# Performance work log

Hardware: AMD Instinct MI355X
Metric: run time of the kernel (lower is better)

The kernel has to match this reference:

```python
import jax, jax.numpy as jnp
import numpy as np

EPS = 1e-5


def _conv1x1(x, w, b):
    # x: (B,C,H,W), w: (O,C), b: (O,)
    return jnp.einsum('oc,bchw->bohw', w, x) + b[None, :, None, None]


def _attn(q, k, v):
    # q,k: (B,Dq,H,W); v: (B,C,H,W). Full NxN attention, softmax over keys.
    B, _, H, W = q.shape
    N = H * W
    Q = q.reshape(B, -1, N)
    K = k.reshape(B, -1, N)
    V = v.reshape(B, -1, N)
    A = jax.nn.softmax(jnp.einsum('bci,bcj->bij', Q, K), axis=-1)  # (B,N,N)
    out = jnp.einsum('bcj,bij->bci', V, A)  # out[b,c,i] = sum_j V[b,c,j] A[b,i,j]
    return out.reshape(B, -1, H, W)


def _std(feat):
    # torch.var(dim=2) is unbiased (ddof=1)
    B, C = feat.shape[:2]
    v = jnp.var(feat.reshape(B, C, -1), axis=2, ddof=1) + EPS
    return jnp.sqrt(v)[:, :, None, None]


def _fmm(fb_feat, bg_feat):
    return fb_feat * (_std(bg_feat) / _std(fb_feat))


def setup_inputs() -> dict:
    key = jax.random.key(0)
    ks = jax.random.split(key, 16)
    B, C, H, W = 2, 256, 64, 64
    D = C // 8
    s = 0.05
    inp = {
        'x': jax.random.normal(ks[0], (B, C, H, W), jnp.float32),
        'mask': jax.random.randint(ks[1], (B, 1, H, W), 0, 2).astype(jnp.float32),
        'sa_wq': jax.random.normal(ks[2], (D, C), jnp.float32) * s,
        'sa_bq': jax.random.normal(ks[3], (D,), jnp.float32) * s,
        'sa_wk': jax.random.normal(ks[4], (D, C), jnp.float32) * s,
        'sa_bk': jax.random.normal(ks[5], (D,), jnp.float32) * s,
        'sa_wv': jax.random.normal(ks[6], (C, C), jnp.float32) * s,
        'sa_bv': jax.random.normal(ks[7], (C,), jnp.float32) * s,
        'sa_gamma': jax.random.uniform(ks[8], (1,), jnp.float32),
        'wq': jax.random.normal(ks[9], (D, C), jnp.float32) * s,
        'bq': jax.random.normal(ks[10], (D,), jnp.float32) * s,
        'wk': jax.random.normal(ks[11], (D, C), jnp.float32) * s,
        'bk': jax.random.normal(ks[12], (D,), jnp.float32) * s,
        'wv': jax.random.normal(ks[13], (C, C), jnp.float32) * s,
        'bv': jax.random.normal(ks[14], (C,), jnp.float32) * s,
        'gamma': jax.random.uniform(ks[15], (1,), jnp.float32),
    }
    return inp


def reference(x, mask, sa_wq, sa_bq, sa_wk, sa_bk, sa_wv, sa_bv, sa_gamma,
              wq, bq, wk, bk, wv, bv, gamma):
    # --- Self_Attn ---
    sa_out = _attn(_conv1x1(x, sa_wq, sa_bq),
                   _conv1x1(x, sa_wk, sa_bk),
                   _conv1x1(x, sa_wv, sa_bv))
    x = sa_gamma[0] * sa_out + x
    # --- FB_FMM masked cross attention (mask already at feature resolution) ---
    reverse_mask = 1.0 - mask
    feature_b = reverse_mask * x
    feature_f = mask * x
    sw_bg = _attn(_conv1x1(feature_f, wq, bq),
                  _conv1x1(feature_b, wk, bk),
                  _conv1x1(feature_b, wv, bv))
    out = x + gamma[0] * _fmm(feature_f, sw_bg)
    return out
```

## Files before the change

kernel.cpp:

```cpp
#include <hip/hip_runtime.h>
#include <stdint.h>

typedef _Float16 f16;
typedef __attribute__((ext_vector_type(8))) _Float16 half8;
typedef __attribute__((ext_vector_type(2))) __fp16 fp16x2;
typedef __attribute__((ext_vector_type(8))) short short8;
typedef __attribute__((ext_vector_type(4))) float f32x4;

#define NPOS 4096
#define CCH  256
#define OQK  64
#define BATCH 2
#define NSPLIT 4
#define KEYS_PER_SPLIT 1024
#define NT (KEYS_PER_SPLIT / 64)

typedef __attribute__((address_space(3))) uint32_t lds_u32;
typedef __attribute__((address_space(1))) const uint32_t glb_u32;

__device__ __forceinline__ float bf2f(short u) {
    union { uint32_t i; float f; } c;
    c.i = ((uint32_t)(uint16_t)u) << 16;
    return c.f;
}
__device__ __forceinline__ short f2bf(float f) {
    union { float f; uint32_t i; } c; c.f = f;
    uint32_t lsb = (c.i >> 16) & 1u;
    c.i += 0x7FFFu + lsb;
    return (short)(c.i >> 16);
}

__device__ __forceinline__ bool detect_bf16(const uint32_t* mw) {
    int hits = 0;
    #pragma unroll
    for (int i = 0; i < 64; ++i) hits += ((mw[i] & 0xFFFFu) == 0x3F80u) ? 1 : 0;
    return hits != 0;
}

__device__ __forceinline__ void load8(const void* base, size_t e0, bool bf, float* v) {
    if (bf) {
        short8 s = *(const short8*)((const short*)base + e0);
        #pragma unroll
        for (int j = 0; j < 8; ++j) v[j] = bf2f(s[j]);
    } else {
        const float* fp = (const float*)base + e0;
        float4 a = *(const float4*)fp;
        float4 b = *(const float4*)(fp + 4);
        v[0] = a.x; v[1] = a.y; v[2] = a.z; v[3] = a.w;
        v[4] = b.x; v[5] = b.y; v[6] = b.z; v[7] = b.w;
    }
}
__device__ __forceinline__ float load1(const void* base, int i, bool bf) {
    return bf ? bf2f(((const short*)base)[i]) : ((const float*)base)[i];
}

__device__ __forceinline__ int pkrtz(float a, float b) {
    union { fp16x2 h; int i; } u;
    u.h = __builtin_amdgcn_cvt_pkrtz(a, b);
    return u.i;
}

__global__ __launch_bounds__(256) void convert_inputs(
    const uint32_t* __restrict__ mask_raw,
    const void* __restrict__ w1q, const void* __restrict__ w1k, const void* __restrict__ w1v_,
    const void* __restrict__ b1q, const void* __restrict__ b1k, const void* __restrict__ b1v_,
    const void* __restrict__ g1,
    const void* __restrict__ w2q, const void* __restrict__ w2k, const void* __restrict__ w2v_,
    const void* __restrict__ b2q, const void* __restrict__ b2k, const void* __restrict__ b2v_,
    const void* __restrict__ g2,
    float* __restrict__ maskf,
    f16* __restrict__ w1qk, f16* __restrict__ w1vm, f16* __restrict__ b1,
    f16* __restrict__ w2qk, f16* __restrict__ w2vm, f16* __restrict__ b2,
    float* __restrict__ gam)
{
    const bool bf = detect_bf16(mask_raw);
    const int blk = blockIdx.x, tid = threadIdx.x;
    float v[8];
    if (blk < 4) {
        const size_t e0 = ((size_t)blk * 256 + tid) * 8;
        load8(mask_raw, e0, bf, v);
        float4 f0 = {v[0], v[1], v[2], v[3]}, f1 = {v[4], v[5], v[6], v[7]};
        *(float4*)(maskf + e0) = f0;
        *(float4*)(maskf + e0 + 4) = f1;
    } else if (blk < 12) {
        const size_t g = ((size_t)(blk - 4) * 256 + tid) * 8;
        const int o = (int)(g >> 8), cc = (int)(g & 255);
        const void* src = (o < 32) ? w1q : w1k;
        const size_t se = (size_t)((o < 32) ? o : o - 32) * 256 + cc;
        load8(src, se, bf, v);
        half8 h;
        #pragma unroll
        for (int j = 0; j < 8; ++j) h[j] = (f16)v[j];
        *(half8*)(w1qk + g) = h;
    } else if (blk < 44) {
        const size_t g = ((size_t)(blk - 12) * 256 + tid) * 8;
        load8(w1v_, g, bf, v);
        half8 h;
        #pragma unroll
        for (int j = 0; j < 8; ++j) h[j] = (f16)v[j];
        *(half8*)(w1vm + g) = h;
    } else if (blk < 52) {
        const size_t g = ((size_t)(blk - 44) * 256 + tid) * 8;
        const int o = (int)(g >> 8), cc = (int)(g & 255);
        const void* src = (o < 32) ? w2q : w2k;
        const size_t se = (size_t)((o < 32) ? o : o - 32) * 256 + cc;
        load8(src, se, bf, v);
        half8 h;
        #pragma unroll
        for (int j = 0; j < 8; ++j) h[j] = (f16)v[j];
        *(half8*)(w2qk + g) = h;
    } else if (blk < 84) {
        const size_t g = ((size_t)(blk - 52) * 256 + tid) * 8;
        load8(w2v_, g, bf, v);
        half8 h;
        #pragma unroll
        for (int j = 0; j < 8; ++j) h[j] = (f16)v[j];
        *(half8*)(w2vm + g) = h;
    } else {
        for (int i = tid; i < 320; i += 256) {
            const void* s1 = (i < 32) ? b1q : (i < 64) ? b1k : b1v_;
            const void* s2 = (i < 32) ? b2q : (i < 64) ? b2k : b2v_;
            const int ii = (i < 32) ? i : (i < 64) ? i - 32 : i - 64;
            b1[i] = (f16)load1(s1, ii, bf);
            b2[i] = (f16)load1(s2, ii, bf);
        }
        if (tid == 0) {
            gam[0] = load1(g1, 0, bf);
            gam[1] = load1(g2, 0, bf);
        }
    }
}

__global__ __launch_bounds__(256) void conv_qkv(
    const void* __restrict__ xin, int is_raw,
    const uint32_t* __restrict__ mask_raw,
    const f16* __restrict__ wqk,
    const f16* __restrict__ wvm,
    const f16* __restrict__ bias,
    const float* __restrict__ maskf, int use_mask,
    f16* __restrict__ qkout,
    f16* __restrict__ vout)
{
    const bool bf = is_raw ? detect_bf16(mask_raw) : false;
    const int b    = blockIdx.y;
    const int n0   = blockIdx.x * 32;
    const int tid  = threadIdx.x;
    const int lane = tid & 63;
    const int w    = tid >> 6;
    const int lo   = lane & 15;
    const int hi   = lane >> 4;

    __shared__ f16 xt[32 * 256];

    {
        const int nc = tid & 3;
        const int cg = tid >> 2;
        #pragma unroll
        for (int it = 0; it < 4; ++it) {
            const int c = cg + 64 * it;
            const size_t off = ((size_t)b * CCH + c) * NPOS + n0 + nc * 8;
            float v8[8];
            load8(xin, off, bf, v8);
            #pragma unroll
            for (int j = 0; j < 8; ++j) {
                const int n = nc * 8 + j;
                int byte = n * 512 + c * 2;
                byte ^= ((n & 7) << 4);
                *(f16*)((char*)xt + byte) = (f16)v8[j];
            }
        }
    }
    __syncthreads();

    const f32x4 z = {0.f, 0.f, 0.f, 0.f};
    f32x4 acc_qk[2];
    f32x4 acc_v[4][2];
    #pragma unroll
    for (int i = 0; i < 2; ++i) {
        acc_qk[i] = z;
        #pragma unroll
        for (int j = 0; j < 4; ++j) acc_v[j][i] = z;
    }

    #pragma unroll 1
    for (int ks = 0; ks < 8; ++ks) {
        const int ce = ks * 32 + 8 * hi;
        half8 xfr[2];
        #pragma unroll
        for (int nt = 0; nt < 2; ++nt) {
            const int n = nt * 16 + lo;
            int byte = n * 512 + ce * 2;
            byte ^= ((n & 7) << 4);
            xfr[nt] = *(const half8*)((const char*)xt + byte);
        }
        {
            half8 wf = *(const half8*)(wqk + (size_t)(w * 16 + lo) * 256 + ce);
            #pragma unroll
            for (int nt = 0; nt < 2; ++nt)
                acc_qk[nt] = __builtin_amdgcn_mfma_f32_16x16x32_f16(xfr[nt], wf, acc_qk[nt], 0, 0, 0);
        }
        #pragma unroll
        for (int ot = 0; ot < 4; ++ot) {
            half8 wf = *(const half8*)(wvm + (size_t)(w * 64 + ot * 16 + lo) * 256 + ce);
            #pragma unroll
            for (int nt = 0; nt < 2; ++nt)
                acc_v[ot][nt] = __builtin_amdgcn_mfma_f32_16x16x32_f16(wf, xfr[nt], acc_v[ot][nt], 0, 0, 0);
        }
    }

    {
        const int o = w * 16 + lo;
        const float bb = (float)bias[o];
        #pragma unroll
        for (int nt = 0; nt < 2; ++nt) {
            #pragma unroll
            for (int r = 0; r < 4; ++r) {
                const int n = n0 + nt * 16 + 4 * hi + r;
                float mult = 1.f;
                if (use_mask) {
                    const float mv = maskf[b * NPOS + n];
                    mult = (o < 32) ? mv : (1.f - mv);
                }
                qkout[((size_t)b * NPOS + n) * OQK + o] = (f16)(mult * acc_qk[nt][r] + bb);
            }
        }
    }
    {
        float mv_n[2];
        #pragma unroll
        for (int nt = 0; nt < 2; ++nt)
            mv_n[nt] = use_mask ? (1.f - maskf[b * NPOS + n0 + nt * 16 + lo]) : 1.f;
        #pragma unroll
        for (int ot = 0; ot < 4; ++ot) {
            #pragma unroll
            for (int r = 0; r < 4; ++r) {
                const int oc = w * 64 + ot * 16 + 4 * hi + r;
                const float bb = (float)bias[64 + oc];
                #pragma unroll
                for (int nt = 0; nt < 2; ++nt) {
                    const int n = n0 + nt * 16 + lo;
                    vout[((size_t)b * CCH + oc) * NPOS + n] = (f16)(mv_n[nt] * acc_v[ot][nt][r] + bb);
                }
            }
        }
    }
}

__global__ __launch_bounds__(512, 4) void attn_split(
    const f16* __restrict__ qk,
    const f16* __restrict__ vbuf,
    f16* __restrict__ po,
    float2* __restrict__ pml)
{
    const int id    = blockIdx.x;
    const int xg    = id & 7;
    const int split = xg & 3;
    const int b     = xg >> 2;
    const int q0    = (id >> 3) * 64;
    const int tid   = threadIdx.x;
    const int lane  = tid & 63;
    const int w     = tid >> 6;
    const int lo    = lane & 15;
    const int hi    = lane >> 4;
    const int qown  = (w & 3) * 16;
    const int cbase = w * 32;

    __shared__ f16 kv[CCH * 64];
    __shared__ f16 kbuf[2][64 * 64];
    __shared__ f16 plds[64 * 64];
    __shared__ float sc_lds[64];
    __shared__ float l_lds[64];
    __shared__ int   flag_lds[4];

    const int trow = tid >> 3;
    const int tch  = tid & 7;

    half8 qfrag;
    if (w < 4)
        qfrag = *(const half8*)(qk + ((size_t)b * NPOS + q0 + qown + lo) * OQK + 8 * hi);

    const f32x4 z = {0.f, 0.f, 0.f, 0.f};
    f32x4 acc[2][4];
    #pragma unroll
    for (int i = 0; i < 2; ++i)
        #pragma unroll
        for (int j = 0; j < 4; ++j) acc[i][j] = z;
    float m_run = -3.0e38f, l_run = 0.f;

    const f16* vsrc = vbuf + (size_t)b * CCH * NPOS;
    const f16* ksrc = qk + (size_t)b * NPOS * OQK;

    #define STAGE_V(kt)                                                        \
    {                                                                          \
        const int j0s = split * KEYS_PER_SPLIT + (kt) * 64;                    \
        _Pragma("unroll")                                                      \
        for (int i = 0; i < 4; ++i) {                                          \
            const int c = i * 64 + trow;                                       \
            const f16* g = vsrc + (size_t)c * NPOS + j0s + ((tch ^ (c & 7)) * 8); \
            char* d = (char*)kv + i * 8192 + w * 1024;                         \
            __builtin_amdgcn_global_load_lds((glb_u32*)g, (lds_u32*)d, 16, 0, 0); \
        }                                                                      \
    }
    #define STAGE_K(kt)                                                        \
    {                                                                          \
        const int j0s = split * KEYS_PER_SPLIT + (kt) * 64;                    \
        char* kb = (char*)kbuf + ((kt) & 1) * 8192;                            \
        const f16* g = ksrc + (size_t)(j0s + trow) * OQK + ((tch ^ (trow & 7)) * 8); \
        __builtin_amdgcn_global_load_lds((glb_u32*)g, (lds_u32*)(kb + w * 1024), 16, 0, 0); \
    }

    STAGE_V(0)
    STAGE_K(0)
    STAGE_K(1)
    asm volatile("s_waitcnt vmcnt(1)" ::: "memory");
    __builtin_amdgcn_s_barrier();
    asm volatile("" ::: "memory");

    #pragma unroll 1
    for (int kt = 0; kt < NT; ++kt) {
        if (w < 4) {
            const char* kb = (const char*)kbuf + (kt & 1) * 8192;
            f32x4 s[4];
            __builtin_amdgcn_s_setprio(1);
            #pragma unroll
            for (int jt = 0; jt < 4; ++jt) {
                const int krow = jt * 16 + lo;
                const half8 kfrag = *(const half8*)(kb + krow * 128
                                                    + ((64 + hi * 16) ^ ((krow & 7) << 4)));
                s[jt] = __builtin_amdgcn_mfma_f32_16x16x32_f16(kfrag, qfrag, z, 0, 0, 0);
            }
            __builtin_amdgcn_s_setprio(0);
            float pm = s[0][0];
            #pragma unroll
            for (int jt = 0; jt < 4; ++jt)
                #pragma unroll
                for (int r = 0; r < 4; ++r) pm = fmaxf(pm, s[jt][r]);
            pm = fmaxf(pm, __shfl_xor(pm, 16, 64));
            pm = fmaxf(pm, __shfl_xor(pm, 32, 64));
            const bool g = __any(pm - m_run > 8.f);
            float scv = 1.f;
            if (g) {
                const float mnew = fmaxf(m_run, pm);
                scv = __expf(m_run - mnew);
                m_run = mnew;
                l_run *= scv;
            }
            float rs = 0.f;
            #pragma unroll
            for (int jt = 0; jt < 4; ++jt) {
                #pragma unroll
                for (int r = 0; r < 4; ++r) {
                    const float pv = __expf(s[jt][r] - m_run);
                    s[jt][r] = pv;
                    rs += pv;
                }
            }
            rs += __shfl_xor(rs, 16, 64);
            rs += __shfl_xor(rs, 32, 64);
            l_run += rs;
            const int q = qown + lo;
            #pragma unroll
            for (int jt = 0; jt < 4; ++jt) {
                union { int i2[2]; uint64_t u; } pw;
                pw.i2[0] = pkrtz(s[jt][0], s[jt][1]);
                pw.i2[1] = pkrtz(s[jt][2], s[jt][3]);
                *(uint64_t*)((char*)plds + q * 128 + ((jt * 32 + 8 * hi) ^ ((q & 7) << 4))) = pw.u;
            }
            if (hi == 0) sc_lds[q] = scv;
            if (lane == 0) flag_lds[w] = g ? 1 : 0;
        }

        asm volatile("s_waitcnt lgkmcnt(0)" ::: "memory");
        if (kt + 1 < NT) {
            asm volatile("s_waitcnt vmcnt(1)" ::: "memory");
        } else {
            asm volatile("s_waitcnt vmcnt(0)" ::: "memory");
        }
        __builtin_amdgcn_sched_barrier(0);
        __builtin_amdgcn_s_barrier();
        asm volatile("" ::: "memory");

        #pragma unroll
        for (int qt = 0; qt < 4; ++qt) {
            if (flag_lds[qt]) {
                const float sc = sc_lds[qt * 16 + lo];
                #pragma unroll
                for (int ct = 0; ct < 2; ++ct) acc[ct][qt] *= sc;
            }
        }
        __builtin_amdgcn_s_setprio(1);
        #pragma unroll
        for (int ksp = 0; ksp < 2; ++ksp) {
            half8 pf[4];
            #pragma unroll
            for (int qt = 0; qt < 4; ++qt)
                pf[qt] = *(const half8*)((const char*)plds + (qt * 16 + lo) * 128
                                         + ((ksp * 64 + 16 * hi) ^ ((lo & 7) << 4)));
            #pragma unroll
            for (int ct = 0; ct < 2; ++ct) {
                const int vrow = cbase + ct * 16 + lo;
                const half8 vf = *(const half8*)((const char*)kv + vrow * 128
                                                 + ((ksp * 64 + 16 * hi) ^ ((vrow & 7) << 4)));
                #pragma unroll
                for (int qt = 0; qt < 4; ++qt)
                    acc[ct][qt] = __builtin_amdgcn_mfma_f32_16x16x32_f16(vf, pf[qt], acc[ct][qt], 0, 0, 0);
            }
        }
        __builtin_amdgcn_s_setprio(0);

        asm volatile("s_waitcnt lgkmcnt(0) vmcnt(0)" ::: "memory");
        __builtin_amdgcn_sched_barrier(0);
        __builtin_amdgcn_s_barrier();
        asm volatile("" ::: "memory");
        if (kt + 1 < NT) STAGE_V(kt + 1)
        if (kt + 2 < NT) STAGE_K(kt + 2)
    }
    #undef STAGE_K
    #undef STAGE_V

    if (w < 4 && hi == 0) {
        l_lds[qown + lo] = l_run;
        float2 v; v.x = m_run; v.y = l_run;
        pml[((size_t)split * BATCH + b) * NPOS + q0 + qown + lo] = v;
    }
    __syncthreads();
    float inv[4];
    #pragma unroll
    for (int qt = 0; qt < 4; ++qt) inv[qt] = 1.f / l_lds[qt * 16 + lo];
    f16* pob = po + (((size_t)split * BATCH + b) * CCH + cbase) * NPOS + q0;
    #pragma unroll
    for (int ct = 0; ct < 2; ++ct) {
        #pragma unroll
        for (int r = 0; r < 4; ++r) {
            const size_t rowo = (size_t)(ct * 16 + 4 * hi + r) * NPOS;
            #pragma unroll
            for (int qt = 0; qt < 4; ++qt)
                pob[rowo + qt * 16 + lo] = (f16)(acc[ct][qt][r] * inv[qt]);
        }
    }
}

__global__ __launch_bounds__(256) void attn_merge(
    const f16* __restrict__ po,
    const float2* __restrict__ pml,
    const void* __restrict__ xraw,
    const uint32_t* __restrict__ mask_raw,
    const float* __restrict__ gamp,
    float* __restrict__ out_f,
    f16* __restrict__ out_h,
    int add_residual)
{
    const int b  = blockIdx.z;
    const int n0 = blockIdx.x * 64;
    const int c0 = blockIdx.y * 32;
    const int tid = threadIdx.x;
    const int cl  = tid >> 3;
    const int oct = tid & 7;

    __shared__ float wls[NSPLIT][64];
    if (tid < 64) {
        const int n = n0 + tid;
        float m[NSPLIT], l[NSPLIT];
        #pragma unroll
        for (int s = 0; s < NSPLIT; ++s) {
            float2 v = pml[((size_t)s * BATCH + b) * NPOS + n];
            m[s] = v.x; l[s] = v.y;
        }
        float M = m[0];
        #pragma unroll
        for (int s = 1; s < NSPLIT; ++s) M = fmaxf(M, m[s]);
        float wgt[NSPLIT], wsum = 0.f;
        #pragma unroll
        for (int s = 0; s < NSPLIT; ++s) { wgt[s] = __expf(m[s] - M) * l[s]; wsum += wgt[s]; }
        const float winv = 1.f / wsum;
        #pragma unroll
        for (int s = 0; s < NSPLIT; ++s) wls[s][tid] = wgt[s] * winv;
    }
    __syncthreads();

    const int c = c0 + cl;
    const int nl = oct * 8;
    const size_t base = ((size_t)b * CCH + c) * NPOS + n0 + nl;
    float o[8] = {0.f, 0.f, 0.f, 0.f, 0.f, 0.f, 0.f, 0.f};
    #pragma unroll
    for (int s = 0; s < NSPLIT; ++s) {
        const half8 pv = *(const half8*)(po + (((size_t)s * BATCH + b) * CCH + c) * NPOS + n0 + nl);
        const float* wr = &wls[s][nl];
        #pragma unroll
        for (int j = 0; j < 8; ++j) o[j] += wr[j] * (float)pv[j];
    }
    if (add_residual) {
        const bool bf = detect_bf16(mask_raw);
        const float gamma = gamp[0];
        float xv[8];
        load8(xraw, base, bf, xv);
        float4 f0, f1;
        f0.x = gamma * o[0] + xv[0]; f0.y = gamma * o[1] + xv[1];
        f0.z = gamma * o[2] + xv[2]; f0.w = gamma * o[3] + xv[3];
        f1.x = gamma * o[4] + xv[4]; f1.y = gamma * o[5] + xv[5];
        f1.z = gamma * o[6] + xv[6]; f1.w = gamma * o[7] + xv[7];
        *(float4*)(out_f + base) = f0;
        *(float4*)(out_f + base + 4) = f1;
    } else {
        half8 h;
        #pragma unroll
        for (int j = 0; j < 8; ++j) h[j] = (f16)o[j];
        *(half8*)(out_h + base) = h;
    }
}

__global__ __launch_bounds__(256) void fmm_final(
    const float* __restrict__ x1f,
    const f16*  __restrict__ bg,
    const float* __restrict__ maskf,
    const float* __restrict__ gamp,
    const uint32_t* __restrict__ mask_raw,
    void* __restrict__ outp)
{
    const bool bf = detect_bf16(mask_raw);
    const int b = blockIdx.y;
    const int c = blockIdx.x;
    const int tid = threadIdx.x;
    const size_t rowoff = ((size_t)b * CCH + c) * NPOS;
    const float* xrow = x1f + rowoff;
    const f16*  grow = bg + rowoff;
    const float* mrow = maskf + (size_t)b * NPOS;

    float s_f = 0.f, ss_f = 0.f, s_g = 0.f, ss_g = 0.f;
    #pragma unroll
    for (int u = 0; u < 2; ++u) {
        const int i = tid * 16 + u * 8;
        const float4 x0 = *(const float4*)(xrow + i);
        const float4 x1v = *(const float4*)(xrow + i + 4);
        const float4 m0 = *(const float4*)(mrow + i);
        const float4 m1 = *(const float4*)(mrow + i + 4);
        half8 gv = *(const half8*)(grow + i);
        const float xs[8] = {x0.x, x0.y, x0.z, x0.w, x1v.x, x1v.y, x1v.z, x1v.w};
        const float ms[8] = {m0.x, m0.y, m0.z, m0.w, m1.x, m1.y, m1.z, m1.w};
        #pragma unroll
        for (int j = 0; j < 8; ++j) {
            const float f = xs[j] * ms[j];
            const float g = (float)gv[j];
            s_f += f; ss_f += f * f;
            s_g += g; ss_g += g * g;
        }
    }
    #pragma unroll
    for (int off = 1; off < 64; off <<= 1) {
        s_f += __shfl_xor(s_f, off, 64);
        ss_f += __shfl_xor(ss_f, off, 64);
        s_g += __shfl_xor(s_g, off, 64);
        ss_g += __shfl_xor(ss_g, off, 64);
    }
    __shared__ float red[4][4];
    const int wv_ = tid >> 6;
    if ((tid & 63) == 0) {
        red[wv_][0] = s_f; red[wv_][1] = ss_f; red[wv_][2] = s_g; red[wv_][3] = ss_g;
    }
    __syncthreads();
    s_f  = red[0][0] + red[1][0] + red[2][0] + red[3][0];
    ss_f = red[0][1] + red[1][1] + red[2][1] + red[3][1];
    s_g  = red[0][2] + red[1][2] + red[2][2] + red[3][2];
    ss_g = red[0][3] + red[1][3] + red[2][3] + red[3][3];

    const float nn = 4096.f, nm1 = 4095.f;
    const float var_f = (ss_f - s_f * s_f / nn) / nm1;
    const float var_g = (ss_g - s_g * s_g / nn) / nm1;
    const float ratio = sqrtf((var_g + 1e-5f) / (var_f + 1e-5f));
    const float gamma = gamp[0];

    #pragma unroll
    for (int u = 0; u < 2; ++u) {
        const int i = tid * 16 + u * 8;
        const float4 x0 = *(const float4*)(xrow + i);
        const float4 x1v = *(const float4*)(xrow + i + 4);
        const float4 m0 = *(const float4*)(mrow + i);
        const float4 m1 = *(const float4*)(mrow + i + 4);
        const float xs[8] = {x0.x, x0.y, x0.z, x0.w, x1v.x, x1v.y, x1v.z, x1v.w};
        const float ms[8] = {m0.x, m0.y, m0.z, m0.w, m1.x, m1.y, m1.z, m1.w};
        float ov[8];
        #pragma unroll
        for (int j = 0; j < 8; ++j)
            ov[j] = xs[j] + gamma * (xs[j] * ms[j]) * ratio;
        if (bf) {
            short8 sv;
            #pragma unroll
            for (int j = 0; j < 8; ++j) sv[j] = f2bf(ov[j]);
            *(short8*)((short*)outp + rowoff + i) = sv;
        } else {
            float4 f0 = {ov[0], ov[1], ov[2], ov[3]}, f1 = {ov[4], ov[5], ov[6], ov[7]};
            *(float4*)((float*)outp + rowoff + i) = f0;
            *(float4*)((float*)outp + rowoff + i + 4) = f1;
        }
    }
}

extern "C" void kernel_launch(void* const* d_in, const int* in_sizes, int n_in,
                              void* d_out, int out_size, void* d_ws, size_t ws_size,
                              hipStream_t stream)
{
    const size_t MB = 1u << 20, KB = 1u << 10;
    char* ws = (char*)d_ws;
    f16*    qkbuf = (f16*)(ws);
    f16*    vbuf  = (f16*)(ws + 1 * MB);
    f16*    bgbuf = (f16*)(ws);
    float*  x1f   = (float*)(ws + 5 * MB);
    f16*    po    = (f16*)(ws + 13 * MB);
    float2* pml   = (float2*)(ws + 29 * MB);
    float*  maskf = (float*)(ws + 29 * MB + 512 * KB);
    f16*    w1qk  = (f16*)(ws + 30 * MB);
    f16*    w1v   = (f16*)(ws + 30 * MB + 32 * KB);
    f16*    b1    = (f16*)(ws + 30 * MB + 160 * KB);
    f16*    w2qk  = (f16*)(ws + 30 * MB + 164 * KB);
    f16*    w2v   = (f16*)(ws + 30 * MB + 196 * KB);
    f16*    b2    = (f16*)(ws + 30 * MB + 324 * KB);
    float*  gam   = (float*)(ws + 30 * MB + 328 * KB);

    const uint32_t* mraw = (const uint32_t*)d_in[1];

    dim3 blk(256);
    dim3 ablk(512);
    dim3 vgrid(85);
    dim3 cgrid(NPOS / 32, BATCH);
    dim3 agrid(NPOS / 64 * NSPLIT * BATCH);
    dim3 mgrid(NPOS / 64, CCH / 32, BATCH);
    dim3 fgrid(CCH, BATCH);

    convert_inputs<<<vgrid, blk, 0, stream>>>(
        mraw,
        d_in[2], d_in[4], d_in[6], d_in[3], d_in[5], d_in[7], d_in[8],
        d_in[9], d_in[11], d_in[13], d_in[10], d_in[12], d_in[14], d_in[15],
        maskf, w1qk, w1v, b1, w2qk, w2v, b2, gam);

    conv_qkv<<<cgrid, blk, 0, stream>>>(d_in[0], 1, mraw, w1qk, w1v, b1, maskf, 0, qkbuf, vbuf);
    attn_split<<<agrid, ablk, 0, stream>>>(qkbuf, vbuf, po, pml);
    attn_merge<<<mgrid, blk, 0, stream>>>(po, pml, d_in[0], mraw, gam + 0, x1f, nullptr, 1);
    conv_qkv<<<cgrid, blk, 0, stream>>>(x1f, 0, mraw, w2qk, w2v, b2, maskf, 1, qkbuf, vbuf);
    attn_split<<<agrid, ablk, 0, stream>>>(qkbuf, vbuf, po, pml);
    attn_merge<<<mgrid, blk, 0, stream>>>(po, pml, nullptr, mraw, gam + 1, nullptr, bgbuf, 0);
    fmm_final<<<fgrid, blk, 0, stream>>>(x1f, bgbuf, maskf, gam + 1, mraw, d_out);
}
```

Measured before the change: 121.5 us.

## Double query tile per attention block so all eight waves compute scores

Raises the attn_split query tile from 64 to 128 rows, so all 8 waves now compute QK scores and softmax instead of only 4, and each wave keeps accumulators for 8 query subtiles. Each staged K/V tile is reused across twice as many queries, which halves global K/V traffic per query and removes idle waves in the score phase. In exchange the accumulator register count doubles, launch bounds drop to 2 blocks per SM, and the grid halves to 512 blocks, which lowers occupancy and parallelism.

```diff
diff --git a/kernel.cpp b/kernel.cpp
--- a/kernel.cpp
+++ b/kernel.cpp
@@ -14,6 +14,7 @@
 #define NSPLIT 4
 #define KEYS_PER_SPLIT 1024
 #define NT (KEYS_PER_SPLIT / 64)
+#define QTILE 128
 
 typedef __attribute__((address_space(3))) uint32_t lds_u32;
 typedef __attribute__((address_space(1))) const uint32_t glb_u32;
@@ -246,7 +247,7 @@
     }
 }
 
-__global__ __launch_bounds__(512, 4) void attn_split(
+__global__ __launch_bounds__(512, 2) void attn_split(
     const f16* __restrict__ qk,
     const f16* __restrict__ vbuf,
     f16* __restrict__ po,
@@ -256,35 +257,33 @@
     const int xg    = id & 7;
     const int split = xg & 3;
     const int b     = xg >> 2;
-    const int q0    = (id >> 3) * 64;
+    const int q0    = (id >> 3) * QTILE;
     const int tid   = threadIdx.x;
     const int lane  = tid & 63;
     const int w     = tid >> 6;
     const int lo    = lane & 15;
     const int hi    = lane >> 4;
-    const int qown  = (w & 3) * 16;
+    const int qown  = w * 16;
     const int cbase = w * 32;
 
     __shared__ f16 kv[CCH * 64];
     __shared__ f16 kbuf[2][64 * 64];
-    __shared__ f16 plds[64 * 64];
-    __shared__ float sc_lds[64];
-    __shared__ float l_lds[64];
-    __shared__ int   flag_lds[4];
+    __shared__ f16 plds[QTILE * 64];
+    __shared__ float sc_lds[QTILE];
+    __shared__ float l_lds[QTILE];
+    __shared__ int   flag_lds[8];
 
     const int trow = tid >> 3;
     const int tch  = tid & 7;
 
-    half8 qfrag;
-    if (w < 4)
-        qfrag = *(const half8*)(qk + ((size_t)b * NPOS + q0 + qown + lo) * OQK + 8 * hi);
+    const half8 qfrag = *(const half8*)(qk + ((size_t)b * NPOS + q0 + qown + lo) * OQK + 8 * hi);
 
     const f32x4 z = {0.f, 0.f, 0.f, 0.f};
-    f32x4 acc[2][4];
+    f32x4 acc[2][8];
     #pragma unroll
     for (int i = 0; i < 2; ++i)
         #pragma unroll
-        for (int j = 0; j < 4; ++j) acc[i][j] = z;
+        for (int j = 0; j < 8; ++j) acc[i][j] = z;
     float m_run = -3.0e38f, l_run = 0.f;
 
     const f16* vsrc = vbuf + (size_t)b * CCH * NPOS;
@@ -318,7 +317,7 @@
 
     #pragma unroll 1
     for (int kt = 0; kt < NT; ++kt) {
-        if (w < 4) {
+        {
             const char* kb = (const char*)kbuf + (kt & 1) * 8192;
             f32x4 s[4];
             __builtin_amdgcn_s_setprio(1);
@@ -381,7 +380,7 @@
         asm volatile("" ::: "memory");
 
         #pragma unroll
-        for (int qt = 0; qt < 4; ++qt) {
+        for (int qt = 0; qt < 8; ++qt) {
             if (flag_lds[qt]) {
                 const float sc = sc_lds[qt * 16 + lo];
                 #pragma unroll
@@ -391,19 +390,17 @@
         __builtin_amdgcn_s_setprio(1);
         #pragma unroll
         for (int ksp = 0; ksp < 2; ++ksp) {
-            half8 pf[4];
-            #pragma unroll
-            for (int qt = 0; qt < 4; ++qt)
-                pf[qt] = *(const half8*)((const char*)plds + (qt * 16 + lo) * 128
-                                         + ((ksp * 64 + 16 * hi) ^ ((lo & 7) << 4)));
             #pragma unroll
             for (int ct = 0; ct < 2; ++ct) {
                 const int vrow = cbase + ct * 16 + lo;
                 const half8 vf = *(const half8*)((const char*)kv + vrow * 128
                                                  + ((ksp * 64 + 16 * hi) ^ ((vrow & 7) << 4)));
                 #pragma unroll
-                for (int qt = 0; qt < 4; ++qt)
-                    acc[ct][qt] = __builtin_amdgcn_mfma_f32_16x16x32_f16(vf, pf[qt], acc[ct][qt], 0, 0, 0);
+                for (int qt = 0; qt < 8; ++qt) {
+                    const half8 pf = *(const half8*)((const char*)plds + (qt * 16 + lo) * 128
+                                                     + ((ksp * 64 + 16 * hi) ^ ((lo & 7) << 4)));
+                    acc[ct][qt] = __builtin_amdgcn_mfma_f32_16x16x32_f16(vf, pf, acc[ct][qt], 0, 0, 0);
+                }
             }
         }
         __builtin_amdgcn_s_setprio(0);
@@ -418,15 +415,15 @@
     #undef STAGE_K
     #undef STAGE_V
 
-    if (w < 4 && hi == 0) {
+    if (hi == 0) {
         l_lds[qown + lo] = l_run;
         float2 v; v.x = m_run; v.y = l_run;
         pml[((size_t)split * BATCH + b) * NPOS + q0 + qown + lo] = v;
     }
     __syncthreads();
-    float inv[4];
-    #pragma unroll
-    for (int qt = 0; qt < 4; ++qt) inv[qt] = 1.f / l_lds[qt * 16 + lo];
+    float inv[8];
+    #pragma unroll
+    for (int qt = 0; qt < 8; ++qt) inv[qt] = 1.f / l_lds[qt * 16 + lo];
     f16* pob = po + (((size_t)split * BATCH + b) * CCH + cbase) * NPOS + q0;
     #pragma unroll
     for (int ct = 0; ct < 2; ++ct) {
@@ -434,7 +431,7 @@
         for (int r = 0; r < 4; ++r) {
             const size_t rowo = (size_t)(ct * 16 + 4 * hi + r) * NPOS;
             #pragma unroll
-            for (int qt = 0; qt < 4; ++qt)
+            for (int qt = 0; qt < 8; ++qt)
                 pob[rowo + qt * 16 + lo] = (f16)(acc[ct][qt][r] * inv[qt]);
         }
     }
@@ -622,7 +619,7 @@
     dim3 ablk(512);
     dim3 vgrid(85);
     dim3 cgrid(NPOS / 32, BATCH);
-    dim3 agrid(NPOS / 64 * NSPLIT * BATCH);
+    dim3 agrid(NPOS / QTILE * NSPLIT * BATCH);
     dim3 mgrid(NPOS / 64, CCH / 32, BATCH);
     dim3 fgrid(CCH, BATCH);
 
```

Result: slower. 135.9 us (+11.9%).

## Fuse split-attention merge into second conv and final FMM kernels

Applied to the files above, without the earlier changes.

Removes both attn_merge kernels. A small wtab_compute kernel now derives the per-query split weights from the (m,l) partials. The first merge and residual add are folded into the load stage of a new conv_qkv_fused kernel. The second merge is recomputed inside fmm_final's statistics pass. This drops the intermediate half-precision background buffer and one round trip of the x1 tensor. In exchange, fmm_final reads all four split partials plus the weight table instead of one merged buffer, and two tiny extra launches are added.

```diff
diff --git a/kernel.cpp b/kernel.cpp
--- a/kernel.cpp
+++ b/kernel.cpp
@@ -131,17 +131,41 @@
     }
 }
 
+__global__ __launch_bounds__(256) void wtab_compute(
+    const float2* __restrict__ pml,
+    float* __restrict__ wtab)
+{
+    const int idx = blockIdx.x * 256 + threadIdx.x;
+    const int b = idx >> 12;
+    const int n = idx & (NPOS - 1);
+    float m[NSPLIT], l[NSPLIT];
+    #pragma unroll
+    for (int s = 0; s < NSPLIT; ++s) {
+        float2 v = pml[((size_t)s * BATCH + b) * NPOS + n];
+        m[s] = v.x; l[s] = v.y;
+    }
+    float M = m[0];
+    #pragma unroll
+    for (int s = 1; s < NSPLIT; ++s) M = fmaxf(M, m[s]);
+    float wgt[NSPLIT], wsum = 0.f;
+    #pragma unroll
+    for (int s = 0; s < NSPLIT; ++s) { wgt[s] = __expf(m[s] - M) * l[s]; wsum += wgt[s]; }
+    const float winv = 1.f / wsum;
+    #pragma unroll
+    for (int s = 0; s < NSPLIT; ++s)
+        wtab[((size_t)s * BATCH + b) * NPOS + n] = wgt[s] * winv;
+}
+
 __global__ __launch_bounds__(256) void conv_qkv(
-    const void* __restrict__ xin, int is_raw,
+    const void* __restrict__ xin,
     const uint32_t* __restrict__ mask_raw,
     const f16* __restrict__ wqk,
     const f16* __restrict__ wvm,
     const f16* __restrict__ bias,
-    const float* __restrict__ maskf, int use_mask,
     f16* __restrict__ qkout,
     f16* __restrict__ vout)
 {
-    const bool bf = is_raw ? detect_bf16(mask_raw) : false;
+    const bool bf = detect_bf16(mask_raw);
     const int b    = blockIdx.y;
     const int n0   = blockIdx.x * 32;
     const int tid  = threadIdx.x;
@@ -216,11 +240,141 @@
             #pragma unroll
             for (int r = 0; r < 4; ++r) {
                 const int n = n0 + nt * 16 + 4 * hi + r;
-                float mult = 1.f;
-                if (use_mask) {
-                    const float mv = maskf[b * NPOS + n];
-                    mult = (o < 32) ? mv : (1.f - mv);
+                qkout[((size_t)b * NPOS + n) * OQK + o] = (f16)(acc_qk[nt][r] + bb);
+            }
+        }
+    }
+    {
+        #pragma unroll
+        for (int ot = 0; ot < 4; ++ot) {
+            #pragma unroll
+            for (int r = 0; r < 4; ++r) {
+                const int oc = w * 64 + ot * 16 + 4 * hi + r;
+                const float bb = (float)bias[64 + oc];
+                #pragma unroll
+                for (int nt = 0; nt < 2; ++nt) {
+                    const int n = n0 + nt * 16 + lo;
+                    vout[((size_t)b * CCH + oc) * NPOS + n] = (f16)(acc_v[ot][nt][r] + bb);
                 }
+            }
+        }
+    }
+}
+
+__global__ __launch_bounds__(256) void conv_qkv_fused(
+    const void* __restrict__ xin,
+    const uint32_t* __restrict__ mask_raw,
+    const f16* __restrict__ po,
+    const float* __restrict__ wtab,
+    const float* __restrict__ gamp,
+    float* __restrict__ x1f,
+    const f16* __restrict__ wqk,
+    const f16* __restrict__ wvm,
+    const f16* __restrict__ bias,
+    const float* __restrict__ maskf,
+    f16* __restrict__ qkout,
+    f16* __restrict__ vout)
+{
+    const bool bf = detect_bf16(mask_raw);
+    const int b    = blockIdx.y;
+    const int n0   = blockIdx.x * 32;
+    const int tid  = threadIdx.x;
+    const int lane = tid & 63;
+    const int w    = tid >> 6;
+    const int lo   = lane & 15;
+    const int hi   = lane >> 4;
+
+    __shared__ f16 xt[32 * 256];
+
+    {
+        const int nc = tid & 3;
+        const int cg = tid >> 2;
+        const float g1 = gamp[0];
+        float wv[NSPLIT][8];
+        #pragma unroll
+        for (int s = 0; s < NSPLIT; ++s) {
+            const float* wb = wtab + ((size_t)s * BATCH + b) * NPOS + n0 + nc * 8;
+            float4 a = *(const float4*)wb;
+            float4 b4 = *(const float4*)(wb + 4);
+            wv[s][0] = a.x; wv[s][1] = a.y; wv[s][2] = a.z; wv[s][3] = a.w;
+            wv[s][4] = b4.x; wv[s][5] = b4.y; wv[s][6] = b4.z; wv[s][7] = b4.w;
+        }
+        #pragma unroll
+        for (int it = 0; it < 4; ++it) {
+            const int c = cg + 64 * it;
+            const size_t off = ((size_t)b * CCH + c) * NPOS + n0 + nc * 8;
+            float v8[8];
+            load8(xin, off, bf, v8);
+            float o[8] = {0.f, 0.f, 0.f, 0.f, 0.f, 0.f, 0.f, 0.f};
+            #pragma unroll
+            for (int s = 0; s < NSPLIT; ++s) {
+                const half8 pv = *(const half8*)(po + (((size_t)s * BATCH + b) * CCH + c) * NPOS + n0 + nc * 8);
+                #pragma unroll
+                for (int j = 0; j < 8; ++j) o[j] += wv[s][j] * (float)pv[j];
+            }
+            float x1[8];
+            #pragma unroll
+            for (int j = 0; j < 8; ++j) x1[j] = g1 * o[j] + v8[j];
+            float4 f0 = {x1[0], x1[1], x1[2], x1[3]}, f1 = {x1[4], x1[5], x1[6], x1[7]};
+            *(float4*)(x1f + off) = f0;
+            *(float4*)(x1f + off + 4) = f1;
+            #pragma unroll
+            for (int j = 0; j < 8; ++j) {
+                const int n = nc * 8 + j;
+                int byte = n * 512 + c * 2;
+                byte ^= ((n & 7) << 4);
+                *(f16*)((char*)xt + byte) = (f16)x1[j];
+            }
+        }
+    }
+    __syncthreads();
+
+    const f32x4 z = {0.f, 0.f, 0.f, 0.f};
+    f32x4 acc_qk[2];
+    f32x4 acc_v[4][2];
+    #pragma unroll
+    for (int i = 0; i < 2; ++i) {
+        acc_qk[i] = z;
+        #pragma unroll
+        for (int j = 0; j < 4; ++j) acc_v[j][i] = z;
+    }
+
+    #pragma unroll 1
+    for (int ks = 0; ks < 8; ++ks) {
+        const int ce = ks * 32 + 8 * hi;
+        half8 xfr[2];
+        #pragma unroll
+        for (int nt = 0; nt < 2; ++nt) {
+            const int n = nt * 16 + lo;
+            int byte = n * 512 + ce * 2;
+            byte ^= ((n & 7) << 4);
+            xfr[nt] = *(const half8*)((const char*)xt + byte);
+        }
+        {
+            half8 wf = *(const half8*)(wqk + (size_t)(w * 16 + lo) * 256 + ce);
+            #pragma unroll
+            for (int nt = 0; nt < 2; ++nt)
+                acc_qk[nt] = __builtin_amdgcn_mfma_f32_16x16x32_f16(xfr[nt], wf, acc_qk[nt], 0, 0, 0);
+        }
+        #pragma unroll
+        for (int ot = 0; ot < 4; ++ot) {
+            half8 wf = *(const half8*)(wvm + (size_t)(w * 64 + ot * 16 + lo) * 256 + ce);
+            #pragma unroll
+            for (int nt = 0; nt < 2; ++nt)
+                acc_v[ot][nt] = __builtin_amdgcn_mfma_f32_16x16x32_f16(wf, xfr[nt], acc_v[ot][nt], 0, 0, 0);
+        }
+    }
+
+    {
+        const int o = w * 16 + lo;
+        const float bb = (float)bias[o];
+        #pragma unroll
+        for (int nt = 0; nt < 2; ++nt) {
+            #pragma unroll
+            for (int r = 0; r < 4; ++r) {
+                const int n = n0 + nt * 16 + 4 * hi + r;
+                const float mv = maskf[b * NPOS + n];
+                const float mult = (o < 32) ? mv : (1.f - mv);
                 qkout[((size_t)b * NPOS + n) * OQK + o] = (f16)(mult * acc_qk[nt][r] + bb);
             }
         }
@@ -229,7 +383,7 @@
         float mv_n[2];
         #pragma unroll
         for (int nt = 0; nt < 2; ++nt)
-            mv_n[nt] = use_mask ? (1.f - maskf[b * NPOS + n0 + nt * 16 + lo]) : 1.f;
+            mv_n[nt] = 1.f - maskf[b * NPOS + n0 + nt * 16 + lo];
         #pragma unroll
         for (int ot = 0; ot < 4; ++ot) {
             #pragma unroll
@@ -440,78 +594,10 @@
     }
 }
 
-__global__ __launch_bounds__(256) void attn_merge(
-    const f16* __restrict__ po,
-    const float2* __restrict__ pml,
-    const void* __restrict__ xraw,
-    const uint32_t* __restrict__ mask_raw,
-    const float* __restrict__ gamp,
-    float* __restrict__ out_f,
-    f16* __restrict__ out_h,
-    int add_residual)
-{
-    const int b  = blockIdx.z;
-    const int n0 = blockIdx.x * 64;
-    const int c0 = blockIdx.y * 32;
-    const int tid = threadIdx.x;
-    const int cl  = tid >> 3;
-    const int oct = tid & 7;
-
-    __shared__ float wls[NSPLIT][64];
-    if (tid < 64) {
-        const int n = n0 + tid;
-        float m[NSPLIT], l[NSPLIT];
-        #pragma unroll
-        for (int s = 0; s < NSPLIT; ++s) {
-            float2 v = pml[((size_t)s * BATCH + b) * NPOS + n];
-            m[s] = v.x; l[s] = v.y;
-        }
-        float M = m[0];
-        #pragma unroll
-        for (int s = 1; s < NSPLIT; ++s) M = fmaxf(M, m[s]);
-        float wgt[NSPLIT], wsum = 0.f;
-        #pragma unroll
-        for (int s = 0; s < NSPLIT; ++s) { wgt[s] = __expf(m[s] - M) * l[s]; wsum += wgt[s]; }
-        const float winv = 1.f / wsum;
-        #pragma unroll
-        for (int s = 0; s < NSPLIT; ++s) wls[s][tid] = wgt[s] * winv;
-    }
-    __syncthreads();
-
-    const int c = c0 + cl;
-    const int nl = oct * 8;
-    const size_t base = ((size_t)b * CCH + c) * NPOS + n0 + nl;
-    float o[8] = {0.f, 0.f, 0.f, 0.f, 0.f, 0.f, 0.f, 0.f};
-    #pragma unroll
-    for (int s = 0; s < NSPLIT; ++s) {
-        const half8 pv = *(const half8*)(po + (((size_t)s * BATCH + b) * CCH + c) * NPOS + n0 + nl);
-        const float* wr = &wls[s][nl];
-        #pragma unroll
-        for (int j = 0; j < 8; ++j) o[j] += wr[j] * (float)pv[j];
-    }
-    if (add_residual) {
-        const bool bf = detect_bf16(mask_raw);
-        const float gamma = gamp[0];
-        float xv[8];
-        load8(xraw, base, bf, xv);
-        float4 f0, f1;
-        f0.x = gamma * o[0] + xv[0]; f0.y = gamma * o[1] + xv[1];
-        f0.z = gamma * o[2] + xv[2]; f0.w = gamma * o[3] + xv[3];
-        f1.x = gamma * o[4] + xv[4]; f1.y = gamma * o[5] + xv[5];
-        f1.z = gamma * o[6] + xv[6]; f1.w = gamma * o[7] + xv[7];
-        *(float4*)(out_f + base) = f0;
-        *(float4*)(out_f + base + 4) = f1;
-    } else {
-        half8 h;
-        #pragma unroll
-        for (int j = 0; j < 8; ++j) h[j] = (f16)o[j];
-        *(half8*)(out_h + base) = h;
-    }
-}
-
 __global__ __launch_bounds__(256) void fmm_final(
     const float* __restrict__ x1f,
-    const f16*  __restrict__ bg,
+    const f16*  __restrict__ po,
+    const float* __restrict__ wtab,
     const float* __restrict__ maskf,
     const float* __restrict__ gamp,
     const uint32_t* __restrict__ mask_raw,
@@ -523,7 +609,6 @@
     const int tid = threadIdx.x;
     const size_t rowoff = ((size_t)b * CCH + c) * NPOS;
     const float* xrow = x1f + rowoff;
-    const f16*  grow = bg + rowoff;
     const float* mrow = maskf + (size_t)b * NPOS;
 
     float s_f = 0.f, ss_f = 0.f, s_g = 0.f, ss_g = 0.f;
@@ -534,15 +619,24 @@
         const float4 x1v = *(const float4*)(xrow + i + 4);
         const float4 m0 = *(const float4*)(mrow + i);
         const float4 m1 = *(const float4*)(mrow + i + 4);
-        half8 gv = *(const half8*)(grow + i);
         const float xs[8] = {x0.x, x0.y, x0.z, x0.w, x1v.x, x1v.y, x1v.z, x1v.w};
         const float ms[8] = {m0.x, m0.y, m0.z, m0.w, m1.x, m1.y, m1.z, m1.w};
+        float gm[8] = {0.f, 0.f, 0.f, 0.f, 0.f, 0.f, 0.f, 0.f};
+        #pragma unroll
+        for (int s = 0; s < NSPLIT; ++s) {
+            const half8 pv = *(const half8*)(po + (((size_t)s * BATCH + b) * CCH + c) * NPOS + i);
+            const float* wb = wtab + ((size_t)s * BATCH + b) * NPOS + i;
+            const float4 wa = *(const float4*)wb;
+            const float4 wb4 = *(const float4*)(wb + 4);
+            const float ws[8] = {wa.x, wa.y, wa.z, wa.w, wb4.x, wb4.y, wb4.z, wb4.w};
+            #pragma unroll
+            for (int j = 0; j < 8; ++j) gm[j] += ws[j] * (float)pv[j];
+        }
         #pragma unroll
         for (int j = 0; j < 8; ++j) {
             const float f = xs[j] * ms[j];
-            const float g = (float)gv[j];
             s_f += f; ss_f += f * f;
-            s_g += g; ss_g += g * g;
+            s_g += gm[j]; ss_g += gm[j] * gm[j];
         }
     }
     #pragma unroll
@@ -603,10 +697,10 @@
     char* ws = (char*)d_ws;
     f16*    qkbuf = (f16*)(ws);
     f16*    vbuf  = (f16*)(ws + 1 * MB);
-    f16*    bgbuf = (f16*)(ws);
     float*  x1f   = (float*)(ws + 5 * MB);
     f16*    po    = (f16*)(ws + 13 * MB);
     float2* pml   = (float2*)(ws + 29 * MB);
+    float*  wtab  = (float*)(ws + 29 * MB + 256 * KB);
     float*  maskf = (float*)(ws + 29 * MB + 512 * KB);
     f16*    w1qk  = (f16*)(ws + 30 * MB);
     f16*    w1v   = (f16*)(ws + 30 * MB + 32 * KB);
@@ -621,9 +715,9 @@
     dim3 blk(256);
     dim3 ablk(512);
     dim3 vgrid(85);
+    dim3 wgrid(32);
     dim3 cgrid(NPOS / 32, BATCH);
     dim3 agrid(NPOS / 64 * NSPLIT * BATCH);
-    dim3 mgrid(NPOS / 64, CCH / 32, BATCH);
     dim3 fgrid(CCH, BATCH);
 
     convert_inputs<<<vgrid, blk, 0, stream>>>(
@@ -632,11 +726,12 @@
         d_in[9], d_in[11], d_in[13], d_in[10], d_in[12], d_in[14], d_in[15],
         maskf, w1qk, w1v, b1, w2qk, w2v, b2, gam);
 
-    conv_qkv<<<cgrid, blk, 0, stream>>>(d_in[0], 1, mraw, w1qk, w1v, b1, maskf, 0, qkbuf, vbuf);
+    conv_qkv<<<cgrid, blk, 0, stream>>>(d_in[0], mraw, w1qk, w1v, b1, qkbuf, vbuf);
     attn_split<<<agrid, ablk, 0, stream>>>(qkbuf, vbuf, po, pml);
-    attn_merge<<<mgrid, blk, 0, stream>>>(po, pml, d_in[0], mraw, gam + 0, x1f, nullptr, 1);
-    conv_qkv<<<cgrid, blk, 0, stream>>>(x1f, 0, mraw, w2qk, w2v, b2, maskf, 1, qkbuf, vbuf);
+    wtab_compute<<<wgrid, blk, 0, stream>>>(pml, wtab);
+    conv_qkv_fused<<<cgrid, blk, 0, stream>>>(d_in[0], mraw, po, wtab, gam + 0, x1f,
+                                              w2qk, w2v, b2, maskf, qkbuf, vbuf);
     attn_split<<<agrid, ablk, 0, stream>>>(qkbuf, vbuf, po, pml);
-    attn_merge<<<mgrid, blk, 0, stream>>>(po, pml, nullptr, mraw, gam + 1, nullptr, bgbuf, 0);
-    fmm_final<<<fgrid, blk, 0, stream>>>(x1f, bgbuf, maskf, gam + 1, mraw, d_out);
-}
+    wtab_compute<<<wgrid, blk, 0, stream>>>(pml, wtab);
+    fmm_final<<<fgrid, blk, 0, stream>>>(x1f, po, wtab, maskf, gam + 1, mraw, d_out);
+}
```

Result: no change. 122.4 us (+0.7%).
